# Optimization experiments

Measured on AMD Instinct MI355X. Metric: run time of the kernel, lower is better.

The kernel has to match this reference:

```python
import jax, jax.numpy as jnp
import numpy as np

C = 512
N_HEADS = 8
K_CH = C // N_HEADS          # 64
ROPE_D = int(K_CH * 0.5)     # 32, only first half of head dim is rotated
ROPE_BASE = 10000


def apply_rope(x):
    # x: [b, h, t, k_ch]; rotate first ROPE_D features, pass the rest through.
    t = x.shape[2]
    d = ROPE_D
    theta = 1.0 / (ROPE_BASE ** (jnp.arange(0, d, 2, dtype=jnp.float32) / d))  # [d/2]
    idx_theta = jnp.arange(t, dtype=jnp.float32)[:, None] * theta[None, :]     # [t, d/2]
    angles = jnp.concatenate([idx_theta, idx_theta], axis=-1)                  # [t, d]
    cos = jnp.cos(angles)[None, None, :, :].astype(x.dtype)
    sin = jnp.sin(angles)[None, None, :, :].astype(x.dtype)
    x_rope, x_pass = x[..., :d], x[..., d:]
    d2 = d // 2
    neg_half = jnp.concatenate([-x_rope[..., d2:], x_rope[..., :d2]], axis=-1)
    x_rope = x_rope * cos + neg_half * sin
    return jnp.concatenate([x_rope, x_pass], axis=-1)


def setup_inputs() -> dict:
    key = jax.random.key(0)
    ks = jax.random.split(key, 9)
    B, T = 16, 1024
    scale = 1.0 / np.sqrt(C)
    return {
        "x": jax.random.normal(ks[0], (B, C, T), dtype=jnp.float32),
        "Wq": jax.random.normal(ks[1], (C, C), dtype=jnp.float32) * scale,
        "bq": jax.random.normal(ks[2], (C,), dtype=jnp.float32) * 0.01,
        "Wk": jax.random.normal(ks[3], (C, C), dtype=jnp.float32) * scale,
        "bk": jax.random.normal(ks[4], (C,), dtype=jnp.float32) * 0.01,
        "Wv": jax.random.normal(ks[5], (C, C), dtype=jnp.float32) * scale,
        "bv": jax.random.normal(ks[6], (C,), dtype=jnp.float32) * 0.01,
        "Wo": jax.random.normal(ks[7], (C, C), dtype=jnp.float32) * scale,
        "bo": jax.random.normal(ks[8], (C,), dtype=jnp.float32) * 0.01,
    }


def reference(x, Wq, bq, Wk, bk, Wv, bv, Wo, bo):
    b, c, t = x.shape
    # 1x1 conv == channel matmul: [o,c] x [b,c,t] -> [b,o,t]
    q = jnp.einsum('oc,bct->bot', Wq, x) + bq[None, :, None]
    k = jnp.einsum('oc,bct->bot', Wk, x) + bk[None, :, None]
    v = jnp.einsum('oc,bct->bot', Wv, x) + bv[None, :, None]

    def to_heads(z):  # [b, c, t] -> [b, h, t, k_ch]
        return z.reshape(b, N_HEADS, K_CH, t).transpose(0, 1, 3, 2)

    q = apply_rope(to_heads(q))
    k = apply_rope(to_heads(k))
    v = to_heads(v)

    # scaled dot product attention (scale = 1/sqrt(head_dim))
    scores = jnp.einsum('bhqd,bhkd->bhqk', q, k) / np.sqrt(K_CH).astype(np.float32)
    attn = jax.nn.softmax(scores, axis=-1)
    out = jnp.einsum('bhqk,bhkd->bhqd', attn, v)  # [b, h, t, k_ch]

    out = out.transpose(0, 1, 3, 2).reshape(b, c, t)  # [b, c, t]
    return jnp.einsum('oc,bct->bot', Wo, out) + bo[None, :, None]
```

## Files before the change

kernel.cpp:

```cpp
#include <hip/hip_runtime.h>
#include <cmath>

#define B_  16
#define T_  1024
#define C_  512
#define NH_ 8
#define HD_ 64

#define AS1 __attribute__((address_space(1)))
#define AS3 __attribute__((address_space(3)))

#define FENCE_VM()   asm volatile("s_waitcnt vmcnt(0)" ::: "memory")
#define FENCE_LGKM() asm volatile("s_waitcnt lgkmcnt(0)" ::: "memory")

typedef __bf16 bf16_t;
typedef __bf16 bf16x8 __attribute__((ext_vector_type(8)));
typedef __bf16 bf16x4 __attribute__((ext_vector_type(4)));
typedef short  shortx8 __attribute__((ext_vector_type(8)));
typedef float  floatx4 __attribute__((ext_vector_type(4)));

__device__ inline float fast_exp2(float x) {
#if __has_builtin(__builtin_amdgcn_exp2f)
  return __builtin_amdgcn_exp2f(x);
#else
  float r; asm("v_exp_f32 %0, %1" : "=v"(r) : "v"(x)); return r;
#endif
}
__device__ inline float hw_sin_rev(float rev) {
  float r; asm("v_sin_f32 %0, %1" : "=v"(r) : "v"(rev)); return r;
}
__device__ inline float hw_cos_rev(float rev) {
  float r; asm("v_cos_f32 %0, %1" : "=v"(r) : "v"(rev)); return r;
}

template <typename V8>
__device__ inline auto mfma_impl(V8 a, V8 b, floatx4 c, int)
    -> decltype(__builtin_amdgcn_mfma_f32_16x16x32_bf16(a, b, c, 0, 0, 0)) {
  return __builtin_amdgcn_mfma_f32_16x16x32_bf16(a, b, c, 0, 0, 0);
}
template <typename V8>
__device__ inline floatx4 mfma_impl(V8 a, V8 b, floatx4 c, long) {
  return __builtin_amdgcn_mfma_f32_16x16x32_bf16(
      __builtin_bit_cast(shortx8, a), __builtin_bit_cast(shortx8, b), c, 0, 0, 0);
}
__device__ inline floatx4 mfma_bf16(bf16x8 a, bf16x8 b, floatx4 c) {
  return mfma_impl(a, b, c, 0);
}

__global__ void convert_weights(const float* __restrict__ w0, const float* __restrict__ w1,
                                const float* __restrict__ w2, const float* __restrict__ w3,
                                bf16_t* __restrict__ d0, bf16_t* __restrict__ d1,
                                bf16_t* __restrict__ d2, bf16_t* __restrict__ d3) {
  const float* s[4] = {w0, w1, w2, w3};
  bf16_t* d[4] = {d0, d1, d2, d3};
  const int which = blockIdx.y;
  int i = blockIdx.x * blockDim.x + threadIdx.x;
  if (i < C_ * C_) d[which][i] = (bf16_t)s[which][i];
}

__global__ void transpose_x(const float* __restrict__ x, bf16_t* __restrict__ xt) {
  __shared__ float tile[32][33];
  const int b = blockIdx.z;
  const int t0 = blockIdx.x * 32, c0 = blockIdx.y * 32;
  const int tx = threadIdx.x, ty = threadIdx.y;
  for (int i = ty; i < 32; i += 8)
    tile[i][tx] = x[((size_t)b * C_ + c0 + i) * T_ + t0 + tx];
  __syncthreads();
  for (int i = ty; i < 32; i += 8)
    xt[((size_t)b * T_ + t0 + i) * C_ + c0 + tx] = (bf16_t)tile[tx][i];
}

__global__ __launch_bounds__(256) void qkv_gemm(
    const bf16_t* __restrict__ Wq, const bf16_t* __restrict__ Wk, const bf16_t* __restrict__ Wv,
    const float* __restrict__ bq, const float* __restrict__ bk, const float* __restrict__ bv,
    const bf16_t* __restrict__ xt,
    bf16_t* __restrict__ qo, bf16_t* __restrict__ ko, bf16_t* __restrict__ vo) {
  const int which = blockIdx.z % 3;
  const int b = blockIdx.z / 3;
  const bf16_t* W = which == 0 ? Wq : (which == 1 ? Wk : Wv);
  const float* bias = which == 0 ? bq : (which == 1 ? bk : bv);
  const int wave = threadIdx.x >> 6, lane = threadIdx.x & 63;
  const int col = lane & 15, quad = lane >> 4;
  const int MbB = blockIdx.y * 128, NbB = blockIdx.x * 128;
  const int Mw = (wave >> 1) * 64, Nw = (wave & 1) * 64;
  const bf16_t* xb = xt + (size_t)b * T_ * C_;

  __shared__ bf16_t As[3][128 * 32];
  __shared__ bf16_t Bs[3][128 * 32];

  auto stageKV = [&](int i) {
    const int k0 = i * 32, buf = i % 3;
#pragma unroll
    for (int c = 0; c < 2; c++) {
      const int j = wave * 128 + c * 64 + lane;
      __builtin_amdgcn_global_load_lds(
          (const AS1 void*)(W + (MbB + (j >> 2)) * C_ + k0 + (j & 3) * 8),
          (AS3 void*)((char*)&As[buf][0] + wave * 2048 + c * 1024), 16, 0, 0);
    }
#pragma unroll
    for (int c = 0; c < 2; c++) {
      const int j = wave * 128 + c * 64 + lane;
      __builtin_amdgcn_global_load_lds(
          (const AS1 void*)(xb + (NbB + (j >> 2)) * C_ + k0 + (j & 3) * 8),
          (AS3 void*)((char*)&Bs[buf][0] + wave * 2048 + c * 1024), 16, 0, 0);
    }
  };

  floatx4 acc[4][4] = {};
  stageKV(0);
  stageKV(1);
  asm volatile("s_waitcnt vmcnt(4)\ns_barrier" ::: "memory");
  for (int i = 0; i < 16; i++) {
    if (i + 2 < 16) stageKV(i + 2);
    const bf16_t* a = &As[i % 3][0];
    const bf16_t* bb = &Bs[i % 3][0];
    bf16x8 af[4], bfr[4];
#pragma unroll
    for (int mi = 0; mi < 4; mi++)
      af[mi] = *(const bf16x8*)(a + (Mw + mi * 16 + col) * 32 + quad * 8);
#pragma unroll
    for (int ni = 0; ni < 4; ni++)
      bfr[ni] = *(const bf16x8*)(bb + (Nw + ni * 16 + col) * 32 + quad * 8);
#pragma unroll
    for (int mi = 0; mi < 4; mi++)
#pragma unroll
      for (int ni = 0; ni < 4; ni++)
        acc[mi][ni] = mfma_bf16(af[mi], bfr[ni], acc[mi][ni]);
    if (i < 14) {
      asm volatile("s_waitcnt vmcnt(4)\ns_barrier" ::: "memory");
    } else if (i == 14) {
      asm volatile("s_waitcnt vmcnt(0)\ns_barrier" ::: "memory");
    }
  }

  const int Mb = MbB + Mw, Nb = NbB + Nw;
#pragma unroll
  for (int mi = 0; mi < 4; mi++)
#pragma unroll
    for (int r = 0; r < 4; r++) {
      const float bval = bias[Mb + mi * 16 + quad * 4 + r];
#pragma unroll
      for (int ni = 0; ni < 4; ni++) acc[mi][ni][r] += bval;
    }

  const int h = Mb >> 6;
  if (which < 2) {
#pragma unroll
    for (int ni = 0; ni < 4; ni++) {
      const int t = Nb + ni * 16 + col;
#pragma unroll
      for (int r = 0; r < 4; r++) {
        const int dd = quad * 4 + r;
        const float theta_rev =
            fast_exp2(-(float)dd * 0.83048202372184059f - 2.6514961294723187f);
        float rev = (float)t * theta_rev;
        rev = rev - floorf(rev);
        const float sn = hw_sin_rev(rev), cs = hw_cos_rev(rev);
        const float a0 = acc[0][ni][r], a1 = acc[1][ni][r];
        acc[0][ni][r] = a0 * cs - a1 * sn;
        acc[1][ni][r] = a1 * cs + a0 * sn;
      }
    }
    bf16_t* out = which == 0 ? qo : ko;
#pragma unroll
    for (int mi = 0; mi < 4; mi++) {
      const int d0 = mi * 16 + quad * 4;
#pragma unroll
      for (int ni = 0; ni < 4; ni++) {
        const int t = Nb + ni * 16 + col;
        bf16x4 pk;
#pragma unroll
        for (int r = 0; r < 4; r++) pk[r] = (bf16_t)acc[mi][ni][r];
        *(bf16x4*)(out + ((size_t)(b * NH_ + h) * T_ + t) * HD_ + d0) = pk;
      }
    }
  } else {
#pragma unroll
    for (int mi = 0; mi < 4; mi++)
#pragma unroll
      for (int ni = 0; ni < 4; ni++) {
        const int t = Nb + ni * 16 + col;
#pragma unroll
        for (int r = 0; r < 4; r++) {
          const int d = mi * 16 + quad * 4 + r;
          vo[((size_t)(b * NH_ + h) * HD_ + d) * T_ + t] = (bf16_t)acc[mi][ni][r];
        }
      }
  }
}

__global__ __launch_bounds__(512) void attn_kernel(
    const bf16_t* __restrict__ qb, const bf16_t* __restrict__ kb,
    const bf16_t* __restrict__ vtb, bf16_t* __restrict__ ob) {
  const int id = blockIdx.x;
  const int bh = id & 127;
  const int qt = id >> 7;
  const int tid = threadIdx.x;
  const int wave = tid >> 6, lane = tid & 63;
  const int col = lane & 15, quad = lane >> 4;
  const int tq0 = qt * 256 + wave * 32;

  const bf16_t* Q = qb + (size_t)bh * T_ * HD_;
  const bf16_t* K = kb + (size_t)bh * T_ * HD_;
  const bf16_t* VT = vtb + (size_t)bh * HD_ * T_;

  __shared__ bf16_t kvs[2][2][4096];
  __shared__ bf16_t pshm[8][32][68];

  auto stage = [&](const char* gRowBase, int rowStrideB, bf16_t* dst) {
    const int r = tid >> 3, ck = tid & 7;
    const char* src = gRowBase + r * rowStrideB + ((ck ^ (r & 7)) << 4);
    __builtin_amdgcn_global_load_lds(
        (const AS1 void*)src,
        (AS3 void*)((char*)dst + wave * 1024), 16, 0, 0);
  };
  auto stageKV = [&](int tk0, int buf) {
    stage((const char*)(K + (size_t)tk0 * HD_), HD_ * 2, &kvs[buf][0][0]);
    stage((const char*)VT + (size_t)tk0 * 2, T_ * 2, &kvs[buf][1][0]);
  };
  auto frag = [&](const bf16_t* base, int R, int cg) -> bf16x8 {
    return *(const bf16x8*)(base + R * 64 + ((cg ^ (R & 7)) << 3));
  };

  floatx4 oacc[2][4] = {};
  floatx4 lacc[2] = {};
  const float CEXP = 0.18033688011112042f;

  bf16x8 ones;
#pragma unroll
  for (int e = 0; e < 8; e++) ones[e] = (bf16_t)1.0f;

  stageKV(0, 0);
  bf16x8 qf[2][2];
#pragma unroll
  for (int g = 0; g < 2; g++)
#pragma unroll
    for (int kk = 0; kk < 2; kk++) {
      bf16x8 raw = *(const bf16x8*)(Q + (tq0 + g * 16 + col) * HD_ + kk * 32 + quad * 8);
#pragma unroll
      for (int e = 0; e < 8; e++) qf[g][kk][e] = (bf16_t)((float)raw[e] * CEXP);
    }
  FENCE_VM();
  __syncthreads();

  for (int it = 0; it < 16; it++) {
    const int buf = it & 1;
    if (it + 1 < 16) stageKV((it + 1) * 64, buf ^ 1);
    const bf16_t* kt = &kvs[buf][0][0];
    const bf16_t* vt = &kvs[buf][1][0];

    floatx4 s[2][4] = {};
#pragma unroll
    for (int ni = 0; ni < 4; ni++)
#pragma unroll
      for (int kk = 0; kk < 2; kk++) {
        const bf16x8 kf = frag(kt, ni * 16 + col, kk * 4 + quad);
        s[0][ni] = mfma_bf16(qf[0][kk], kf, s[0][ni]);
        s[1][ni] = mfma_bf16(qf[1][kk], kf, s[1][ni]);
      }

#pragma unroll
    for (int g = 0; g < 2; g++)
#pragma unroll
      for (int ni = 0; ni < 4; ni++)
#pragma unroll
        for (int r = 0; r < 4; r++) {
          pshm[wave][g * 16 + quad * 4 + r][ni * 16 + col] = (bf16_t)fast_exp2(s[g][ni][r]);
        }
    FENCE_LGKM();
#pragma unroll
    for (int kk = 0; kk < 2; kk++) {
      bf16x8 pf[2];
#pragma unroll
      for (int g = 0; g < 2; g++)
        pf[g] = *(const bf16x8*)(&pshm[wave][g * 16 + col][kk * 32 + quad * 8]);
#pragma unroll
      for (int nd = 0; nd < 4; nd++) {
        const bf16x8 vf = frag(vt, nd * 16 + col, kk * 4 + quad);
        oacc[0][nd] = mfma_bf16(pf[0], vf, oacc[0][nd]);
        oacc[1][nd] = mfma_bf16(pf[1], vf, oacc[1][nd]);
      }
      lacc[0] = mfma_bf16(pf[0], ones, lacc[0]);
      lacc[1] = mfma_bf16(pf[1], ones, lacc[1]);
    }
    FENCE_VM();
    __syncthreads();
  }

  float linv[2][4];
#pragma unroll
  for (int g = 0; g < 2; g++)
#pragma unroll
    for (int r = 0; r < 4; r++) linv[g][r] = 1.0f / lacc[g][r];
#pragma unroll
  for (int g = 0; g < 2; g++)
#pragma unroll
    for (int nd = 0; nd < 4; nd++)
#pragma unroll
      for (int r = 0; r < 4; r++) {
        const float v = oacc[g][nd][r] * linv[g][r];
        ob[((size_t)bh * T_ + tq0 + g * 16 + quad * 4 + r) * HD_ + nd * 16 + col] = (bf16_t)v;
      }
}

__global__ __launch_bounds__(256) void out_gemm(
    const bf16_t* __restrict__ W, const float* __restrict__ bias,
    const bf16_t* __restrict__ ao, float* __restrict__ y) {
  const int b = blockIdx.z;
  const int wave = threadIdx.x >> 6, lane = threadIdx.x & 63;
  const int col = lane & 15, quad = lane >> 4;
  const int MbB = blockIdx.y * 128, NbB = blockIdx.x * 128;
  const int Mw = (wave >> 1) * 64, Nw = (wave & 1) * 64;
  const bf16_t* ab = ao + (size_t)b * NH_ * T_ * HD_;

  __shared__ bf16_t As[3][128 * 32];
  __shared__ bf16_t Bs[3][128 * 32];

  auto stageKV = [&](int i) {
    const int k0 = i * 32, buf = i % 3;
#pragma unroll
    for (int c = 0; c < 2; c++) {
      const int j = wave * 128 + c * 64 + lane;
      __builtin_amdgcn_global_load_lds(
          (const AS1 void*)(W + (MbB + (j >> 2)) * C_ + k0 + (j & 3) * 8),
          (AS3 void*)((char*)&As[buf][0] + wave * 2048 + c * 1024), 16, 0, 0);
    }
#pragma unroll
    for (int c = 0; c < 2; c++) {
      const int j = wave * 128 + c * 64 + lane;
      const int kg = k0 + (j & 3) * 8;
      __builtin_amdgcn_global_load_lds(
          (const AS1 void*)(ab + ((size_t)(kg >> 6) * T_ + NbB + (j >> 2)) * HD_ + (kg & 63)),
          (AS3 void*)((char*)&Bs[buf][0] + wave * 2048 + c * 1024), 16, 0, 0);
    }
  };

  floatx4 acc[4][4] = {};
  stageKV(0);
  stageKV(1);
  asm volatile("s_waitcnt vmcnt(4)\ns_barrier" ::: "memory");
  for (int i = 0; i < 16; i++) {
    if (i + 2 < 16) stageKV(i + 2);
    const bf16_t* a = &As[i % 3][0];
    const bf16_t* bb = &Bs[i % 3][0];
    bf16x8 af[4], bfr[4];
#pragma unroll
    for (int mi = 0; mi < 4; mi++)
      af[mi] = *(const bf16x8*)(a + (Mw + mi * 16 + col) * 32 + quad * 8);
#pragma unroll
    for (int ni = 0; ni < 4; ni++)
      bfr[ni] = *(const bf16x8*)(bb + (Nw + ni * 16 + col) * 32 + quad * 8);
#pragma unroll
    for (int mi = 0; mi < 4; mi++)
#pragma unroll
      for (int ni = 0; ni < 4; ni++)
        acc[mi][ni] = mfma_bf16(af[mi], bfr[ni], acc[mi][ni]);
    if (i < 14) {
      asm volatile("s_waitcnt vmcnt(4)\ns_barrier" ::: "memory");
    } else if (i == 14) {
      asm volatile("s_waitcnt vmcnt(0)\ns_barrier" ::: "memory");
    }
  }

  const int Mb = MbB + Mw, Nb = NbB + Nw;
#pragma unroll
  for (int mi = 0; mi < 4; mi++)
#pragma unroll
    for (int r = 0; r < 4; r++) {
      const int o = Mb + mi * 16 + quad * 4 + r;
      const float bval = bias[o];
#pragma unroll
      for (int ni = 0; ni < 4; ni++) {
        const int t = Nb + ni * 16 + col;
        y[((size_t)b * C_ + o) * T_ + t] = acc[mi][ni][r] + bval;
      }
    }
}

extern "C" void kernel_launch(void* const* d_in, const int* in_sizes, int n_in,
                              void* d_out, int out_size, void* d_ws, size_t ws_size,
                              hipStream_t stream) {
  const float* x  = (const float*)d_in[0];
  const float* Wq = (const float*)d_in[1];
  const float* bq = (const float*)d_in[2];
  const float* Wk = (const float*)d_in[3];
  const float* bk = (const float*)d_in[4];
  const float* Wv = (const float*)d_in[5];
  const float* bv = (const float*)d_in[6];
  const float* Wo = (const float*)d_in[7];
  const float* bo = (const float*)d_in[8];
  float* y = (float*)d_out;

  char* ws = (char*)d_ws;
  const size_t WB = (size_t)C_ * C_ * 2;
  const size_t XB = (size_t)B_ * T_ * C_ * 2;
  bf16_t* wqb = (bf16_t*)(ws + 0 * WB);
  bf16_t* wkb = (bf16_t*)(ws + 1 * WB);
  bf16_t* wvb = (bf16_t*)(ws + 2 * WB);
  bf16_t* wob = (bf16_t*)(ws + 3 * WB);
  bf16_t* xt  = (bf16_t*)(ws + 4 * WB);
  bf16_t* qb_ = (bf16_t*)(ws + 4 * WB + 1 * XB);
  bf16_t* kb_ = (bf16_t*)(ws + 4 * WB + 2 * XB);
  bf16_t* vtb = (bf16_t*)(ws + 4 * WB + 3 * XB);
  bf16_t* aob = xt;

  convert_weights<<<dim3(1024, 4), dim3(256), 0, stream>>>(
      Wq, Wk, Wv, Wo, wqb, wkb, wvb, wob);
  transpose_x<<<dim3(T_ / 32, C_ / 32, B_), dim3(32, 8), 0, stream>>>(x, xt);
  qkv_gemm<<<dim3(T_ / 128, C_ / 128, B_ * 3), dim3(256), 0, stream>>>(
      wqb, wkb, wvb, bq, bk, bv, xt, qb_, kb_, vtb);
  attn_kernel<<<dim3((T_ / 256) * B_ * NH_), dim3(512), 0, stream>>>(qb_, kb_, vtb, aob);
  out_gemm<<<dim3(T_ / 128, C_ / 128, B_), dim3(256), 0, stream>>>(wob, bo, aob, y);
}
```

Baseline: 210.9 us.

## Keep softmax probabilities in registers by transposing QK MFMA operands

Swaps the A/B operands of the QK^T MFMA so each lane holds score values in the layout needed as the A operand of a 16x16x16 MFMA for the PV product. This removes the per-wave LDS round-trip for the probability tile and its lgkm wait. Row sums are now accumulated in VALU and reduced with cross-lane shuffles instead of extra MFMAs against a ones vector. It also adds an occupancy hint to launch_bounds. In exchange, PV uses twice as many smaller-K MFMAs and narrower V fragment loads from LDS.

New measurement: 205.7 us. -2.5%, faster.

```diff
diff --git a/kernel.cpp b/kernel.cpp
--- a/kernel.cpp
+++ b/kernel.cpp
@@ -17,6 +17,7 @@
 typedef __bf16 bf16x8 __attribute__((ext_vector_type(8)));
 typedef __bf16 bf16x4 __attribute__((ext_vector_type(4)));
 typedef short  shortx8 __attribute__((ext_vector_type(8)));
+typedef short  shortx4 __attribute__((ext_vector_type(4)));
 typedef float  floatx4 __attribute__((ext_vector_type(4)));
 
 __device__ inline float fast_exp2(float x) {
@@ -45,6 +46,18 @@
 }
 __device__ inline floatx4 mfma_bf16(bf16x8 a, bf16x8 b, floatx4 c) {
   return mfma_impl(a, b, c, 0);
+}
+
+__device__ inline floatx4 mfma16_bf16(bf16x4 a, bf16x4 b, floatx4 c) {
+#if __has_builtin(__builtin_amdgcn_mfma_f32_16x16x16bf16_1k)
+  return __builtin_amdgcn_mfma_f32_16x16x16bf16_1k(
+      __builtin_bit_cast(shortx4, a), __builtin_bit_cast(shortx4, b), c, 0, 0, 0);
+#else
+  floatx4 d;
+  asm("v_mfma_f32_16x16x16_bf16 %0, %1, %2, %3"
+      : "=v"(d) : "v"(a), "v"(b), "0"(c));
+  return d;
+#endif
 }
 
 __global__ void convert_weights(const float* __restrict__ w0, const float* __restrict__ w1,
@@ -189,7 +202,7 @@
   }
 }
 
-__global__ __launch_bounds__(512) void attn_kernel(
+__global__ __launch_bounds__(512, 4) void attn_kernel(
     const bf16_t* __restrict__ qb, const bf16_t* __restrict__ kb,
     const bf16_t* __restrict__ vtb, bf16_t* __restrict__ ob) {
   const int id = blockIdx.x;
@@ -205,7 +218,6 @@
   const bf16_t* VT = vtb + (size_t)bh * HD_ * T_;
 
   __shared__ bf16_t kvs[2][2][4096];
-  __shared__ bf16_t pshm[8][32][68];
 
   auto stage = [&](const char* gRowBase, int rowStrideB, bf16_t* dst) {
     const int r = tid >> 3, ck = tid & 7;
@@ -223,12 +235,8 @@
   };
 
   floatx4 oacc[2][4] = {};
-  floatx4 lacc[2] = {};
+  floatx4 lacc4[2] = {};
   const float CEXP = 0.18033688011112042f;
-
-  bf16x8 ones;
-#pragma unroll
-  for (int e = 0; e < 8; e++) ones[e] = (bf16_t)1.0f;
 
   stageKV(0, 0);
   bf16x8 qf[2][2];
@@ -255,43 +263,55 @@
 #pragma unroll
       for (int kk = 0; kk < 2; kk++) {
         const bf16x8 kf = frag(kt, ni * 16 + col, kk * 4 + quad);
-        s[0][ni] = mfma_bf16(qf[0][kk], kf, s[0][ni]);
-        s[1][ni] = mfma_bf16(qf[1][kk], kf, s[1][ni]);
-      }
-
+        s[0][ni] = mfma_bf16(kf, qf[0][kk], s[0][ni]);
+        s[1][ni] = mfma_bf16(kf, qf[1][kk], s[1][ni]);
+      }
+
+    bf16x4 p4[2][4];
 #pragma unroll
     for (int g = 0; g < 2; g++)
 #pragma unroll
       for (int ni = 0; ni < 4; ni++)
 #pragma unroll
         for (int r = 0; r < 4; r++) {
-          pshm[wave][g * 16 + quad * 4 + r][ni * 16 + col] = (bf16_t)fast_exp2(s[g][ni][r]);
+          const float pv = fast_exp2(s[g][ni][r]);
+          lacc4[g][r] += pv;
+          p4[g][ni][r] = (bf16_t)pv;
         }
-    FENCE_LGKM();
-#pragma unroll
-    for (int kk = 0; kk < 2; kk++) {
-      bf16x8 pf[2];
-#pragma unroll
-      for (int g = 0; g < 2; g++)
-        pf[g] = *(const bf16x8*)(&pshm[wave][g * 16 + col][kk * 32 + quad * 8]);
-#pragma unroll
-      for (int nd = 0; nd < 4; nd++) {
-        const bf16x8 vf = frag(vt, nd * 16 + col, kk * 4 + quad);
-        oacc[0][nd] = mfma_bf16(pf[0], vf, oacc[0][nd]);
-        oacc[1][nd] = mfma_bf16(pf[1], vf, oacc[1][nd]);
-      }
-      lacc[0] = mfma_bf16(pf[0], ones, lacc[0]);
-      lacc[1] = mfma_bf16(pf[1], ones, lacc[1]);
-    }
+
+#pragma unroll
+    for (int nd = 0; nd < 4; nd++) {
+      const int R = nd * 16 + col;
+      bf16x4 v4[4];
+#pragma unroll
+      for (int ni = 0; ni < 4; ni++) {
+        const int c8 = ni * 2 + (quad >> 1);
+        v4[ni] = *(const bf16x4*)(vt + R * 64 + ((c8 ^ (R & 7)) << 3) + (quad & 1) * 4);
+      }
+#pragma unroll
+      for (int ni = 0; ni < 4; ni++) {
+        oacc[0][nd] = mfma16_bf16(p4[0][ni], v4[ni], oacc[0][nd]);
+        oacc[1][nd] = mfma16_bf16(p4[1][ni], v4[ni], oacc[1][nd]);
+      }
+    }
+
     FENCE_VM();
     __syncthreads();
   }
 
+  float lrow[2];
+#pragma unroll
+  for (int g = 0; g < 2; g++) {
+    lrow[g] = lacc4[g][0] + lacc4[g][1] + lacc4[g][2] + lacc4[g][3];
+    lrow[g] += __shfl_xor(lrow[g], 16, 64);
+    lrow[g] += __shfl_xor(lrow[g], 32, 64);
+  }
   float linv[2][4];
 #pragma unroll
   for (int g = 0; g < 2; g++)
 #pragma unroll
-    for (int r = 0; r < 4; r++) linv[g][r] = 1.0f / lacc[g][r];
+    for (int r = 0; r < 4; r++)
+      linv[g][r] = 1.0f / __shfl(lrow[g], quad * 4 + r, 64);
 #pragma unroll
   for (int g = 0; g < 2; g++)
 #pragma unroll
```
